# Optimization experiments

Hardware: AMD Instinct MI355X
Metric: run time of the kernel (lower is better)

Reference implementation:

```python
import jax, jax.numpy as jnp
import numpy as np

B, S, H = 16, 8192, 512

def setup_inputs() -> dict:
    key = jax.random.key(0)
    k1, k2, k3, k4, k5 = jax.random.split(key, 5)
    scale = 1.0 / np.sqrt(H)
    return {
        "encoder_outputs": jax.random.normal(k1, (B, S, H), dtype=jnp.float32),
        "query": jax.random.normal(k2, (B, H), dtype=jnp.float32),
        "W_h": jax.random.normal(k3, (H, H), dtype=jnp.float32) * scale,
        "W_q": jax.random.normal(k4, (H, H), dtype=jnp.float32) * scale,
        "v": jax.random.normal(k5, (H,), dtype=jnp.float32) * scale,
    }

def reference(encoder_outputs, query, W_h, W_q, v):
    # h_proj: (B,S,H) = enc @ W_h^T (torch Linear convention)
    h_proj = jnp.einsum('bsh,oh->bso', encoder_outputs, W_h)
    # q_proj: (B,1,H)
    q_proj = jnp.einsum('bh,oh->bo', query, W_q)[:, None, :]
    # scores: (B,S) = tanh(h_proj + q_proj) @ v
    scores = jnp.einsum('bso,o->bs', jnp.tanh(h_proj + q_proj), v)
    alpha = jax.nn.softmax(scores, axis=1)          # (B,S)
    context = jnp.einsum('bs,bsh->bh', alpha, encoder_outputs)  # (B,H)
    return (context, alpha)
```

## Files before the change

### kernel.cpp

```cpp
#include <hip/hip_runtime.h>

typedef float  f32x4  __attribute__((ext_vector_type(4)));
typedef __bf16 bf16x8 __attribute__((ext_vector_type(8)));

#define LOG2E      1.4426950408889634f
#define TWO_LOG2E  2.8853900817779268f

__device__ __forceinline__ float fast_tanh(float x) {
    float e = __builtin_amdgcn_exp2f(x * TWO_LOG2E);
    return 1.0f - 2.0f * __builtin_amdgcn_rcpf(e + 1.0f);
}

__device__ __forceinline__ int a_chunk(int m, int k8) {
    return (((m >> 4) * 16 + (k8 >> 2)) << 6) +
           ((((k8 & 3) << 4) | (m & 15)) ^ ((k8 >> 2) & 7) ^ (((k8 & 3) << 1) & 7));
}

__global__ void wh_swizzle_kernel(const float* __restrict__ Wh,
                                  __bf16* __restrict__ Wswz) {
    int gid = blockIdx.x * 256 + threadIdx.x;
    int n   = gid >> 6;
    int k8  = gid & 63;
    const float* g = Wh + ((long)n << 9) + (k8 << 3);
    f32x4 f0 = *(const f32x4*)g;
    f32x4 f1 = *(const f32x4*)(g + 4);
    bf16x8 val;
    val[0] = (__bf16)f0[0]; val[1] = (__bf16)f0[1];
    val[2] = (__bf16)f0[2]; val[3] = (__bf16)f0[3];
    val[4] = (__bf16)f1[0]; val[5] = (__bf16)f1[1];
    val[6] = (__bf16)f1[2]; val[7] = (__bf16)f1[3];
    int chunk = (((n >> 4) * 16 + (k8 >> 2)) << 6) + (((k8 & 3) << 4) | (n & 15));
    *(bf16x8*)(Wswz + ((long)chunk << 3)) = val;
}

__global__ void qproj_kernel(const float* __restrict__ query,
                             const float* __restrict__ Wq,
                             float* __restrict__ qp) {
    int pair = (blockIdx.x << 2) + (threadIdx.x >> 6);
    int l    = threadIdx.x & 63;
    int b    = pair >> 9;
    long o   = pair & 511;
    const f32x4* q  = (const f32x4*)(query + (b << 9) + (l << 3));
    const f32x4* wr = (const f32x4*)(Wq + (o << 9) + (l << 3));
    f32x4 a0 = q[0], a1 = q[1], w0 = wr[0], w1 = wr[1];
    float acc = a0[0]*w0[0] + a0[1]*w0[1] + a0[2]*w0[2] + a0[3]*w0[3]
              + a1[0]*w1[0] + a1[1]*w1[1] + a1[2]*w1[2] + a1[3]*w1[3];
    #pragma unroll
    for (int off = 1; off < 64; off <<= 1) acc += __shfl_xor(acc, off, 64);
    if (l == 0) qp[pair] = acc;
}

__global__ __launch_bounds__(512, 4) void score_ctx_kernel(
    const float*  __restrict__ enc,
    const __bf16* __restrict__ Wswz,
    const float*  __restrict__ qp,
    const float*  __restrict__ v,
    float* __restrict__ alpha_out,
    float* __restrict__ ctx_acc,
    float* __restrict__ denom)
{
    __shared__ __align__(16) unsigned char ldsA[65536];
    __shared__ float score_lds[512];
    __shared__ float escore[64];

    const int  t    = threadIdx.x;
    const int  w    = t >> 6;
    const int  l    = t & 63;
    const long row0 = (long)blockIdx.x << 6;
    const int  b    = (int)(row0 >> 13);

    f32x4 acc[4][4];
    float vv[4];
    #pragma unroll
    for (int nt = 0; nt < 4; ++nt) {
        int n = (w << 6) + (nt << 4) + (l & 15);
        float q = qp[(b << 9) + n];
        vv[nt] = v[n];
        f32x4 qv = {q, q, q, q};
        #pragma unroll
        for (int mt = 0; mt < 4; ++mt) acc[nt][mt] = qv;
    }

    #pragma unroll
    for (int i = 0; i < 8; ++i) {
        int cflat = t + (i << 9);
        int m = cflat >> 6, k8 = cflat & 63;
        const float* g = enc + ((row0 + m) << 9) + (k8 << 3);
        f32x4 f0 = *(const f32x4*)g;
        f32x4 f1 = *(const f32x4*)(g + 4);
        bf16x8 val;
        val[0] = (__bf16)f0[0]; val[1] = (__bf16)f0[1];
        val[2] = (__bf16)f0[2]; val[3] = (__bf16)f0[3];
        val[4] = (__bf16)f1[0]; val[5] = (__bf16)f1[1];
        val[6] = (__bf16)f1[2]; val[7] = (__bf16)f1[3];
        *(bf16x8*)(ldsA + (a_chunk(m, k8) << 4)) = val;
    }

    __syncthreads();

    const bf16x8* Bg = (const bf16x8*)Wswz;
    #pragma unroll 2
    for (int s = 0; s < 16; ++s) {
        bf16x8 af[4];
        int lowr = l ^ (s & 7) ^ (((l >> 4) << 1) & 7);
        #pragma unroll
        for (int mt = 0; mt < 4; ++mt)
            af[mt] = *(const bf16x8*)(ldsA + (((((mt << 4) + s) << 6) + lowr) << 4));
        #pragma unroll
        for (int nt = 0; nt < 4; ++nt) {
            bf16x8 bf = Bg[((((w << 2) + nt) * 16 + s) << 6) + l];
            #pragma unroll
            for (int mt = 0; mt < 4; ++mt)
                acc[nt][mt] = __builtin_amdgcn_mfma_f32_16x16x32_bf16(
                    af[mt], bf, acc[nt][mt], 0, 0, 0);
        }
    }

    float srow[16];
    #pragma unroll
    for (int i = 0; i < 16; ++i) srow[i] = 0.f;
    #pragma unroll
    for (int nt = 0; nt < 4; ++nt) {
        float vn = vv[nt];
        #pragma unroll
        for (int mt = 0; mt < 4; ++mt)
            #pragma unroll
            for (int r = 0; r < 4; ++r)
                srow[mt * 4 + r] += vn * fast_tanh(acc[nt][mt][r]);
    }
    #pragma unroll
    for (int i = 0; i < 16; ++i) {
        #pragma unroll
        for (int off = 1; off < 16; off <<= 1)
            srow[i] += __shfl_xor(srow[i], off, 64);
    }
    if ((l & 15) == 0) {
        int qd = l >> 4;
        #pragma unroll
        for (int mt = 0; mt < 4; ++mt)
            #pragma unroll
            for (int r = 0; r < 4; ++r)
                score_lds[(w << 6) + (mt << 4) + (qd << 2) + r] = srow[mt * 4 + r];
    }
    __syncthreads();

    if (t < 64) {
        float sc = 0.f;
        #pragma unroll
        for (int ww = 0; ww < 8; ++ww) sc += score_lds[(ww << 6) + t];
        float e = __builtin_amdgcn_exp2f(sc * LOG2E);
        alpha_out[row0 + t] = e;
        escore[t] = e;
        float ssum = e;
        #pragma unroll
        for (int off = 1; off < 64; off <<= 1) ssum += __shfl_xor(ssum, off, 64);
        if (t == 0) atomicAdd(denom + b, ssum);
    }
    __syncthreads();

    float ca[8];
    #pragma unroll
    for (int j = 0; j < 8; ++j) ca[j] = 0.f;
    #pragma unroll
    for (int ii = 0; ii < 8; ++ii) {
        int m = (w << 3) + ii;
        float em = escore[m];
        bf16x8 av = *(const bf16x8*)(ldsA + (a_chunk(m, l) << 4));
        #pragma unroll
        for (int j = 0; j < 8; ++j) ca[j] += em * (float)av[j];
    }
    __syncthreads();
    float* part = (float*)ldsA;
    #pragma unroll
    for (int j = 0; j < 8; ++j) part[t * 9 + j] = ca[j];
    __syncthreads();
    {
        int h = t;
        int k8h = h >> 3, j = h & 7;
        float sum = 0.f;
        #pragma unroll
        for (int rg = 0; rg < 8; ++rg) sum += part[((rg << 6) | k8h) * 9 + j];
        atomicAdd(ctx_acc + ((long)b << 9) + h, sum);
    }
}

__global__ void normalize_kernel(const float* __restrict__ ctx_acc,
                                 const float* __restrict__ denom,
                                 float* __restrict__ out) {
    int i = blockIdx.x * 256 + threadIdx.x;
    if (i < 8192) {
        int b = i >> 9;
        out[i] = ctx_acc[i] / denom[b];
    } else if (i < 8192 + 131072) {
        int b = (i - 8192) >> 13;
        out[i] = out[i] / denom[b];
    }
}

extern "C" void kernel_launch(void* const* d_in, const int* in_sizes, int n_in,
                              void* d_out, int out_size, void* d_ws, size_t ws_size,
                              hipStream_t stream) {
    const float* enc   = (const float*)d_in[0];
    const float* query = (const float*)d_in[1];
    const float* Wh    = (const float*)d_in[2];
    const float* Wq    = (const float*)d_in[3];
    const float* v     = (const float*)d_in[4];
    float* out = (float*)d_out;

    char* ws = (char*)d_ws;
    float*  ctx_acc = (float*)ws;
    float*  denom   = (float*)(ws + 32768);
    float*  qp      = (float*)(ws + 32832);
    __bf16* Wswz    = (__bf16*)(ws + 65600);

    hipMemsetAsync(ws, 0, 32832, stream);
    wh_swizzle_kernel<<<128, 256, 0, stream>>>(Wh, Wswz);
    qproj_kernel<<<2048, 256, 0, stream>>>(query, Wq, qp);
    score_ctx_kernel<<<2048, 512, 0, stream>>>(enc, Wswz, qp, v,
                                               out + 8192, ctx_acc, denom);
    normalize_kernel<<<544, 256, 0, stream>>>(ctx_acc, denom, out);
}
```

Measured before the change: 424.5 us.

## Warp-specialize score kernel with producer waves double-buffering encoder tiles

Restructures the score/context kernel so each block handles 512 rows in 8 iterations. Four producer waves prefetch and convert the next 64-row encoder tile into a second LDS buffer while eight consumer waves run MFMAs on the current one. The consumer loop also register-prefetches the next W_h fragments and accumulates the context and softmax denominator across iterations, so each block issues fewer atomics. In exchange, LDS use doubles to 128KB, which limits residency to one block per CU. Only 256 blocks are launched, and producers hold 32 f32x4 values in registers each.

Result: slower. 695.6 us (+63.9%).

```diff
diff --git a/kernel.cpp b/kernel.cpp
--- a/kernel.cpp
+++ b/kernel.cpp
@@ -5,6 +5,8 @@
 
 #define LOG2E      1.4426950408889634f
 #define TWO_LOG2E  2.8853900817779268f
+
+#define BAR_LDS() asm volatile("s_waitcnt lgkmcnt(0)\n\ts_barrier" ::: "memory")
 
 __device__ __forceinline__ float fast_tanh(float x) {
     float e = __builtin_amdgcn_exp2f(x * TWO_LOG2E);
@@ -14,6 +16,13 @@
 __device__ __forceinline__ int a_chunk(int m, int k8) {
     return (((m >> 4) * 16 + (k8 >> 2)) << 6) +
            ((((k8 & 3) << 4) | (m & 15)) ^ ((k8 >> 2) & 7) ^ (((k8 & 3) << 1) & 7));
+}
+
+__device__ __forceinline__ bf16x8 cvt_chunk(f32x4 f0, f32x4 f1) {
+    bf16x8 val;
+    val[0]=(__bf16)f0[0]; val[1]=(__bf16)f0[1]; val[2]=(__bf16)f0[2]; val[3]=(__bf16)f0[3];
+    val[4]=(__bf16)f1[0]; val[5]=(__bf16)f1[1]; val[6]=(__bf16)f1[2]; val[7]=(__bf16)f1[3];
+    return val;
 }
 
 __global__ void wh_swizzle_kernel(const float* __restrict__ Wh,
@@ -22,13 +31,7 @@
     int n   = gid >> 6;
     int k8  = gid & 63;
     const float* g = Wh + ((long)n << 9) + (k8 << 3);
-    f32x4 f0 = *(const f32x4*)g;
-    f32x4 f1 = *(const f32x4*)(g + 4);
-    bf16x8 val;
-    val[0] = (__bf16)f0[0]; val[1] = (__bf16)f0[1];
-    val[2] = (__bf16)f0[2]; val[3] = (__bf16)f0[3];
-    val[4] = (__bf16)f1[0]; val[5] = (__bf16)f1[1];
-    val[6] = (__bf16)f1[2]; val[7] = (__bf16)f1[3];
+    bf16x8 val = cvt_chunk(*(const f32x4*)g, *(const f32x4*)(g + 4));
     int chunk = (((n >> 4) * 16 + (k8 >> 2)) << 6) + (((k8 & 3) << 4) | (n & 15));
     *(bf16x8*)(Wswz + ((long)chunk << 3)) = val;
 }
@@ -50,7 +53,7 @@
     if (l == 0) qp[pair] = acc;
 }
 
-__global__ __launch_bounds__(512, 4) void score_ctx_kernel(
+__global__ __launch_bounds__(768, 3) void score_ctx_kernel(
     const float*  __restrict__ enc,
     const __bf16* __restrict__ Wswz,
     const float*  __restrict__ qp,
@@ -59,128 +62,180 @@
     float* __restrict__ ctx_acc,
     float* __restrict__ denom)
 {
-    __shared__ __align__(16) unsigned char ldsA[65536];
+    __shared__ __align__(16) unsigned char ldsA[2][65536];
     __shared__ float score_lds[512];
     __shared__ float escore[64];
 
     const int  t    = threadIdx.x;
+    const bool cons = (t < 512);
     const int  w    = t >> 6;
     const int  l    = t & 63;
-    const long row0 = (long)blockIdx.x << 6;
-    const int  b    = (int)(row0 >> 13);
-
-    f32x4 acc[4][4];
-    float vv[4];
-    #pragma unroll
-    for (int nt = 0; nt < 4; ++nt) {
-        int n = (w << 6) + (nt << 4) + (l & 15);
-        float q = qp[(b << 9) + n];
-        vv[nt] = v[n];
-        f32x4 qv = {q, q, q, q};
-        #pragma unroll
-        for (int mt = 0; mt < 4; ++mt) acc[nt][mt] = qv;
-    }
-
-    #pragma unroll
-    for (int i = 0; i < 8; ++i) {
-        int cflat = t + (i << 9);
-        int m = cflat >> 6, k8 = cflat & 63;
-        const float* g = enc + ((row0 + m) << 9) + (k8 << 3);
-        f32x4 f0 = *(const f32x4*)g;
-        f32x4 f1 = *(const f32x4*)(g + 4);
-        bf16x8 val;
-        val[0] = (__bf16)f0[0]; val[1] = (__bf16)f0[1];
-        val[2] = (__bf16)f0[2]; val[3] = (__bf16)f0[3];
-        val[4] = (__bf16)f1[0]; val[5] = (__bf16)f1[1];
-        val[6] = (__bf16)f1[2]; val[7] = (__bf16)f1[3];
-        *(bf16x8*)(ldsA + (a_chunk(m, k8) << 4)) = val;
-    }
-
-    __syncthreads();
-
-    const bf16x8* Bg = (const bf16x8*)Wswz;
-    #pragma unroll 2
-    for (int s = 0; s < 16; ++s) {
-        bf16x8 af[4];
-        int lowr = l ^ (s & 7) ^ (((l >> 4) << 1) & 7);
-        #pragma unroll
-        for (int mt = 0; mt < 4; ++mt)
-            af[mt] = *(const bf16x8*)(ldsA + (((((mt << 4) + s) << 6) + lowr) << 4));
+    const int  p    = t - 512;
+    const long rowB = (long)blockIdx.x << 9;
+    const int  b    = (int)(rowB >> 13);
+
+    float qv[4], vv[4];
+    if (cons) {
         #pragma unroll
         for (int nt = 0; nt < 4; ++nt) {
-            bf16x8 bf = Bg[((((w << 2) + nt) * 16 + s) << 6) + l];
-            #pragma unroll
-            for (int mt = 0; mt < 4; ++mt)
-                acc[nt][mt] = __builtin_amdgcn_mfma_f32_16x16x32_bf16(
-                    af[mt], bf, acc[nt][mt], 0, 0, 0);
-        }
-    }
-
-    float srow[16];
-    #pragma unroll
-    for (int i = 0; i < 16; ++i) srow[i] = 0.f;
-    #pragma unroll
-    for (int nt = 0; nt < 4; ++nt) {
-        float vn = vv[nt];
-        #pragma unroll
-        for (int mt = 0; mt < 4; ++mt)
-            #pragma unroll
-            for (int r = 0; r < 4; ++r)
-                srow[mt * 4 + r] += vn * fast_tanh(acc[nt][mt][r]);
-    }
-    #pragma unroll
-    for (int i = 0; i < 16; ++i) {
-        #pragma unroll
-        for (int off = 1; off < 16; off <<= 1)
-            srow[i] += __shfl_xor(srow[i], off, 64);
-    }
-    if ((l & 15) == 0) {
-        int qd = l >> 4;
-        #pragma unroll
-        for (int mt = 0; mt < 4; ++mt)
-            #pragma unroll
-            for (int r = 0; r < 4; ++r)
-                score_lds[(w << 6) + (mt << 4) + (qd << 2) + r] = srow[mt * 4 + r];
-    }
-    __syncthreads();
-
-    if (t < 64) {
-        float sc = 0.f;
-        #pragma unroll
-        for (int ww = 0; ww < 8; ++ww) sc += score_lds[(ww << 6) + t];
-        float e = __builtin_amdgcn_exp2f(sc * LOG2E);
-        alpha_out[row0 + t] = e;
-        escore[t] = e;
-        float ssum = e;
-        #pragma unroll
-        for (int off = 1; off < 64; off <<= 1) ssum += __shfl_xor(ssum, off, 64);
-        if (t == 0) atomicAdd(denom + b, ssum);
-    }
-    __syncthreads();
+            int n = (w << 6) + (nt << 4) + (l & 15);
+            qv[nt] = qp[(b << 9) + n];
+            vv[nt] = v[n];
+        }
+    }
+
+    if (!cons) {
+        f32x4 g0[16], g1[16];
+        #pragma unroll
+        for (int j = 0; j < 16; ++j) {
+            int cflat = p + (j << 8);
+            int m = cflat >> 6, k8 = cflat & 63;
+            const float* g = enc + ((rowB + m) << 9) + (k8 << 3);
+            g0[j] = *(const f32x4*)g;
+            g1[j] = *(const f32x4*)(g + 4);
+        }
+        #pragma unroll
+        for (int j = 0; j < 16; ++j) {
+            int cflat = p + (j << 8);
+            int m = cflat >> 6, k8 = cflat & 63;
+            *(bf16x8*)(ldsA[0] + (a_chunk(m, k8) << 4)) = cvt_chunk(g0[j], g1[j]);
+        }
+    }
+    BAR_LDS();
 
     float ca[8];
     #pragma unroll
     for (int j = 0; j < 8; ++j) ca[j] = 0.f;
-    #pragma unroll
-    for (int ii = 0; ii < 8; ++ii) {
-        int m = (w << 3) + ii;
-        float em = escore[m];
-        bf16x8 av = *(const bf16x8*)(ldsA + (a_chunk(m, l) << 4));
-        #pragma unroll
-        for (int j = 0; j < 8; ++j) ca[j] += em * (float)av[j];
-    }
-    __syncthreads();
+    float dsum = 0.f;
+    const bf16x8* Bg = (const bf16x8*)Wswz;
+
+    for (int i = 0; i < 8; ++i) {
+        const int  cur  = i & 1;
+        const long row0 = rowB + (i << 6);
+
+        f32x4 pg0[16], pg1[16];
+        if (!cons) {
+            if (i < 7) {
+                const float* encN = enc + ((row0 + 64) << 9);
+                #pragma unroll
+                for (int j = 0; j < 16; ++j) {
+                    int cflat = p + (j << 8);
+                    int m = cflat >> 6, k8 = cflat & 63;
+                    const float* g = encN + ((long)m << 9) + (k8 << 3);
+                    pg0[j] = *(const f32x4*)g;
+                    pg1[j] = *(const f32x4*)(g + 4);
+                }
+            }
+        } else {
+            f32x4 acc[4][4];
+            #pragma unroll
+            for (int nt = 0; nt < 4; ++nt) {
+                f32x4 qvv = {qv[nt], qv[nt], qv[nt], qv[nt]};
+                #pragma unroll
+                for (int mt = 0; mt < 4; ++mt) acc[nt][mt] = qvv;
+            }
+            const int bbase = (w << 12) + l;
+            const unsigned char* lbase = ldsA[cur];
+            bf16x8 bcur[4], bnxt[4];
+            #pragma unroll
+            for (int nt = 0; nt < 4; ++nt) bcur[nt] = Bg[bbase + (nt << 10)];
+            #pragma unroll
+            for (int s = 0; s < 16; ++s) {
+                if (s < 15) {
+                    #pragma unroll
+                    for (int nt = 0; nt < 4; ++nt)
+                        bnxt[nt] = Bg[bbase + (nt << 10) + ((s + 1) << 6)];
+                }
+                int lowr = l ^ (s & 7) ^ (((l >> 4) << 1) & 7);
+                bf16x8 af[4];
+                #pragma unroll
+                for (int mt = 0; mt < 4; ++mt)
+                    af[mt] = *(const bf16x8*)(lbase + (((((mt << 4) + s) << 6) + lowr) << 4));
+                #pragma unroll
+                for (int nt = 0; nt < 4; ++nt)
+                    #pragma unroll
+                    for (int mt = 0; mt < 4; ++mt)
+                        acc[nt][mt] = __builtin_amdgcn_mfma_f32_16x16x32_bf16(
+                            af[mt], bcur[nt], acc[nt][mt], 0, 0, 0);
+                #pragma unroll
+                for (int nt = 0; nt < 4; ++nt) bcur[nt] = bnxt[nt];
+            }
+            float srow[16];
+            #pragma unroll
+            for (int q = 0; q < 16; ++q) srow[q] = 0.f;
+            #pragma unroll
+            for (int nt = 0; nt < 4; ++nt) {
+                float vn = vv[nt];
+                #pragma unroll
+                for (int mt = 0; mt < 4; ++mt)
+                    #pragma unroll
+                    for (int r = 0; r < 4; ++r)
+                        srow[mt * 4 + r] += vn * fast_tanh(acc[nt][mt][r]);
+            }
+            #pragma unroll
+            for (int q = 0; q < 16; ++q) {
+                #pragma unroll
+                for (int off = 1; off < 16; off <<= 1)
+                    srow[q] += __shfl_xor(srow[q], off, 64);
+            }
+            if ((l & 15) == 0) {
+                int qd = l >> 4;
+                #pragma unroll
+                for (int mt = 0; mt < 4; ++mt)
+                    #pragma unroll
+                    for (int r = 0; r < 4; ++r)
+                        score_lds[(w << 6) + (mt << 4) + (qd << 2) + r] = srow[mt * 4 + r];
+            }
+        }
+        BAR_LDS();
+
+        if (cons && t < 64) {
+            float sc = 0.f;
+            #pragma unroll
+            for (int ww = 0; ww < 8; ++ww) sc += score_lds[(ww << 6) + t];
+            float e = __builtin_amdgcn_exp2f(sc * LOG2E);
+            alpha_out[row0 + t] = e;
+            escore[t] = e;
+            float ssum = e;
+            #pragma unroll
+            for (int off = 1; off < 64; off <<= 1) ssum += __shfl_xor(ssum, off, 64);
+            dsum += ssum;
+        }
+        BAR_LDS();
+
+        if (cons) {
+            #pragma unroll
+            for (int ii = 0; ii < 8; ++ii) {
+                int m = (w << 3) + ii;
+                float em = escore[m];
+                bf16x8 av = *(const bf16x8*)(ldsA[cur] + (a_chunk(m, l) << 4));
+                #pragma unroll
+                for (int j = 0; j < 8; ++j) ca[j] += em * (float)av[j];
+            }
+        } else if (i < 7) {
+            #pragma unroll
+            for (int j = 0; j < 16; ++j) {
+                int cflat = p + (j << 8);
+                int m = cflat >> 6, k8 = cflat & 63;
+                *(bf16x8*)(ldsA[1 - cur] + (a_chunk(m, k8) << 4)) = cvt_chunk(pg0[j], pg1[j]);
+            }
+        }
+        BAR_LDS();
+    }
+
     float* part = (float*)ldsA;
-    #pragma unroll
-    for (int j = 0; j < 8; ++j) part[t * 9 + j] = ca[j];
-    __syncthreads();
-    {
-        int h = t;
-        int k8h = h >> 3, j = h & 7;
+    if (cons) {
+        #pragma unroll
+        for (int j = 0; j < 8; ++j) part[t * 9 + j] = ca[j];
+    }
+    BAR_LDS();
+    if (cons) {
+        int h = t, k8h = h >> 3, j = h & 7;
         float sum = 0.f;
         #pragma unroll
         for (int rg = 0; rg < 8; ++rg) sum += part[((rg << 6) | k8h) * 9 + j];
         atomicAdd(ctx_acc + ((long)b << 9) + h, sum);
+        if (t == 0) atomicAdd(denom + b, dsum);
     }
 }
 
@@ -216,7 +271,7 @@
     hipMemsetAsync(ws, 0, 32832, stream);
     wh_swizzle_kernel<<<128, 256, 0, stream>>>(Wh, Wswz);
     qproj_kernel<<<2048, 256, 0, stream>>>(query, Wq, qp);
-    score_ctx_kernel<<<2048, 512, 0, stream>>>(enc, Wswz, qp, v,
-                                               out + 8192, ctx_acc, denom);
+    score_ctx_kernel<<<256, 768, 0, stream>>>(enc, Wswz, qp, v,
+                                              out + 8192, ctx_acc, denom);
     normalize_kernel<<<544, 256, 0, stream>>>(ctx_acc, denom, out);
 }
```
